# Performance work log

Hardware: AMD Instinct MI355X
Metric: run time of the kernel (lower is better)

The kernel has to match this reference:

```python
import jax, jax.numpy as jnp
import numpy as np

B, S, D, H = 2, 2048, 1024, 16
HD = D // H  # head_dim = 64


def setup_inputs() -> dict:
    key = jax.random.key(0)
    ks = jax.random.split(key, 9)
    s_in = 1.0 / np.sqrt(D)
    inp = {
        "hidden_state": jax.random.normal(ks[0], (B, S, D), dtype=jnp.float32),
        # per-head projections, stacked: [H, D, HD]
        "Wq": jax.random.uniform(ks[1], (H, D, HD), jnp.float32, -s_in, s_in),
        "bq": jax.random.uniform(ks[2], (H, HD), jnp.float32, -s_in, s_in),
        "Wk": jax.random.uniform(ks[3], (H, D, HD), jnp.float32, -s_in, s_in),
        "bk": jax.random.uniform(ks[4], (H, HD), jnp.float32, -s_in, s_in),
        "Wv": jax.random.uniform(ks[5], (H, D, HD), jnp.float32, -s_in, s_in),
        "bv": jax.random.uniform(ks[6], (H, HD), jnp.float32, -s_in, s_in),
        # output linear: [D, D]
        "Wo": jax.random.uniform(ks[7], (D, D), jnp.float32, -s_in, s_in),
        "bo": jax.random.uniform(ks[8], (D,), jnp.float32, -s_in, s_in),
    }
    return inp


def reference(hidden_state, Wq, bq, Wk, bk, Wv, bv, Wo, bo):
    # fused per-head projections: [B, H, S, HD]
    q = jnp.einsum("bsd,hde->bhse", hidden_state, Wq) + bq[None, :, None, :]
    k = jnp.einsum("bsd,hde->bhse", hidden_state, Wk) + bk[None, :, None, :]
    v = jnp.einsum("bsd,hde->bhse", hidden_state, Wv) + bv[None, :, None, :]
    scale = 1.0 / jnp.sqrt(jnp.float32(HD))
    scores = jnp.einsum("bhse,bhte->bhst", q, k) * scale  # [B, H, S, S]
    weights = jax.nn.softmax(scores, axis=-1)
    ctx = jnp.einsum("bhst,bhte->bhse", weights, v)       # [B, H, S, HD]
    # concat heads along last dim -> [B, S, D]
    ctx = jnp.transpose(ctx, (0, 2, 1, 3)).reshape(B, S, D)
    return ctx @ Wo + bo
```

## Files before the change

kernel.cpp:

```cpp
#include <hip/hip_runtime.h>
#include <hip/hip_bf16.h>
#include <math.h>

#define BB 2
#define SS 2048
#define DD 1024
#define HH 16
#define HD 64

typedef __attribute__((ext_vector_type(8))) _Float16 f16x8;
typedef __attribute__((ext_vector_type(2))) __fp16 fp16x2;
typedef __attribute__((ext_vector_type(8))) unsigned short u16x8;
typedef __attribute__((ext_vector_type(4))) float f32x4;
typedef __attribute__((ext_vector_type(4))) unsigned short u16x4;

__device__ __forceinline__ unsigned short hbits(_Float16 h) {
    union { _Float16 h; unsigned short s; } u; u.h = h; return u.s;
}

__device__ __forceinline__ int swz(int row, int grp) {
    return (row << 6) + (((grp) ^ (row & 7)) << 3);
}

__device__ __forceinline__ float fexp2(float x) {
#if __has_builtin(__builtin_amdgcn_exp2f)
    return __builtin_amdgcn_exp2f(x);
#else
    return exp2f(x);
#endif
}

__device__ __forceinline__ u16x4 pack4(float p0, float p1, float p2, float p3) {
#if __has_builtin(__builtin_amdgcn_cvt_pkrtz)
    union { fp16x2 h[2]; u16x4 u; } pu;
    pu.h[0] = __builtin_amdgcn_cvt_pkrtz(p0, p1);
    pu.h[1] = __builtin_amdgcn_cvt_pkrtz(p2, p3);
    return pu.u;
#else
    u16x4 r;
    r[0] = hbits((_Float16)p0); r[1] = hbits((_Float16)p1);
    r[2] = hbits((_Float16)p2); r[3] = hbits((_Float16)p3);
    return r;
#endif
}

__device__ __forceinline__ void gload_lds16(const unsigned short* g, unsigned short* l) {
#if __has_builtin(__builtin_amdgcn_global_load_lds)
    auto gp = (const __attribute__((address_space(1))) unsigned int*)(uintptr_t)g;
    auto lp = (__attribute__((address_space(3))) unsigned int*)(uintptr_t)l;
    __builtin_amdgcn_global_load_lds(gp, lp, 16, 0, 0);
#else
    *(u16x8*)(l + (threadIdx.x & 63) * 8) = *(const u16x8*)g;
#endif
}

__device__ __forceinline__ void wait4_barrier() {
    asm volatile("s_waitcnt vmcnt(4) lgkmcnt(0)\n\ts_barrier" ::: "memory");
}
__device__ __forceinline__ void wait6_barrier() {
    asm volatile("s_waitcnt vmcnt(6) lgkmcnt(0)\n\ts_barrier" ::: "memory");
}
__device__ __forceinline__ void wait0_barrier() {
    asm volatile("s_waitcnt vmcnt(0) lgkmcnt(0)\n\ts_barrier" ::: "memory");
}

__global__ __launch_bounds__(256) void prep_convert(
    const float* __restrict__ X,
    const float* __restrict__ Wq, const float* __restrict__ Wk,
    const float* __restrict__ Wv, const float* __restrict__ Wo,
    unsigned short* __restrict__ Xh, unsigned short* __restrict__ WT)
{
    __shared__ __align__(16) unsigned short LT[64 * 68];
    const int bid = blockIdx.x;
    const int tid = threadIdx.x;

    if (bid < 2048) {
        const int base = bid * 2048 + tid * 8;
        float4 a = *(const float4*)&X[base];
        float4 b = *(const float4*)&X[base + 4];
        u16x8 o;
        o[0] = hbits((_Float16)a.x); o[1] = hbits((_Float16)a.y);
        o[2] = hbits((_Float16)a.z); o[3] = hbits((_Float16)a.w);
        o[4] = hbits((_Float16)b.x); o[5] = hbits((_Float16)b.y);
        o[6] = hbits((_Float16)b.z); o[7] = hbits((_Float16)b.w);
        *(u16x8*)&Xh[base] = o;
        return;
    }

    const int t = bid - 2048;
    const float* src;
    size_t stride;
    int outRow0, kcol0;
    if (t < 768) {
        const int nt = t >> 4, ktile = t & 15;
        const int sel = nt >> 4, hh = nt & 15;
        const float* Ws = (sel == 0) ? Wq : ((sel == 1) ? Wk : Wv);
        src = Ws + (size_t)hh * (DD * HD) + (size_t)ktile * 64 * HD;
        stride = HD;
        outRow0 = nt * 64;
        kcol0 = ktile * 64;
    } else {
        const int tt = t - 768;
        const int nt = tt & 15, ktile = tt >> 4;
        src = Wo + (size_t)ktile * 64 * DD + nt * 64;
        stride = DD;
        outRow0 = 3072 + nt * 64;
        kcol0 = ktile * 64;
    }

    const int e = tid & 63, dq = tid >> 6;
#pragma unroll
    for (int p = 0; p < 16; p++) {
        const int dl = p * 4 + dq;
        LT[e * 68 + dl] = hbits((_Float16)src[(size_t)dl * stride + e]);
    }
    __syncthreads();
    const int eo = tid >> 2, d16 = (tid & 3) * 16;
#pragma unroll
    for (int j = 0; j < 4; j++) {
        *(ushort4*)&WT[(size_t)(outRow0 + eo) * DD + kcol0 + d16 + j * 4] =
            *(const ushort4*)&LT[eo * 68 + d16 + j * 4];
    }
}

#define GBM 128
#define GBN 128
#define GBK 64
#define NKT (DD / GBK)
#define QBK 32
#define QNKT (DD / QBK)

__global__ __launch_bounds__(256) void qkv_gemm(
    const unsigned short* __restrict__ Xh, const unsigned short* __restrict__ WT,
    const float* __restrict__ bq, const float* __restrict__ bk,
    const float* __restrict__ bv,
    unsigned short* __restrict__ qh, unsigned short* __restrict__ kh,
    unsigned short* __restrict__ vTs, unsigned int* __restrict__ kc2)
{
    __shared__ __align__(16) unsigned short As[3][8 * 512];
    __shared__ __align__(16) unsigned short Bs[3][8 * 512];

    const int tid = threadIdx.x;
    const int f  = blockIdx.y * 24 + blockIdx.x;
    const int fs = (f & 7) * 96 + (f >> 3);
    const int bx = fs % 24, by = fs / 24;
    const int m0 = by * GBM;
    const int n0 = bx * GBN;
    const int lane = tid & 63;
    const int w = tid >> 6;
    const int wm = w & 1, wn = w >> 1;
    const int l15 = lane & 15, quad = lane >> 4;
    const int kstart = (fs * 7) & (QNKT - 1);

    int g_off[2];
#pragma unroll
    for (int p = 0; p < 2; p++) {
        const int c = p * 4 + w;
        g_off[p] = (c * 16 + l15) * DD + quad * 8;
    }

    f32x4 acc[4][4];
#pragma unroll
    for (int i = 0; i < 4; i++)
#pragma unroll
        for (int j = 0; j < 4; j++) acc[i][j] = (f32x4){0.f, 0.f, 0.f, 0.f};

    const unsigned short* Abase = Xh + (size_t)m0 * DD;
    const unsigned short* Bbase = WT + (size_t)n0 * DD;

    {
        const int k0 = kstart * QBK;
        const int k1 = ((kstart + 1) & (QNKT - 1)) * QBK;
#pragma unroll
        for (int p = 0; p < 2; p++) {
            gload_lds16(Abase + g_off[p] + k0, &As[0][(p * 4 + w) * 512]);
            gload_lds16(Bbase + g_off[p] + k0, &Bs[0][(p * 4 + w) * 512]);
        }
#pragma unroll
        for (int p = 0; p < 2; p++) {
            gload_lds16(Abase + g_off[p] + k1, &As[1][(p * 4 + w) * 512]);
            gload_lds16(Bbase + g_off[p] + k1, &Bs[1][(p * 4 + w) * 512]);
        }
    }
    wait0_barrier();

    int cur = 0, pre = 2;
    for (int t = 0; t < QNKT; t++) {
        if (t + 2 < QNKT) {
            const int kt2 = ((kstart + t + 2) & (QNKT - 1)) * QBK;
#pragma unroll
            for (int p = 0; p < 2; p++) {
                gload_lds16(Abase + g_off[p] + kt2, &As[pre][(p * 4 + w) * 512]);
                gload_lds16(Bbase + g_off[p] + kt2, &Bs[pre][(p * 4 + w) * 512]);
            }
        }
        f16x8 af[4], bf[4];
#pragma unroll
        for (int i = 0; i < 4; i++) {
            af[i] = *(const f16x8*)&As[cur][(wm * 4 + i) * 512 + lane * 8];
            bf[i] = *(const f16x8*)&Bs[cur][(wn * 4 + i) * 512 + lane * 8];
        }
#pragma unroll
        for (int ns = 0; ns < 4; ns++)
#pragma unroll
            for (int ms = 0; ms < 4; ms++)
                acc[ms][ns] = __builtin_amdgcn_mfma_f32_16x16x32_f16(
                    af[ms], bf[ns], acc[ms][ns], 0, 0, 0);
        if (t < QNKT - 2)       wait4_barrier();
        else if (t == QNKT - 2) wait0_barrier();
        cur = (cur == 2) ? 0 : cur + 1;
        pre = (pre == 2) ? 0 : pre + 1;
    }

    const int sel = n0 >> 10;
    const int hw = ((n0 + wn * 64) >> 6) & 15;
    const int bblk = m0 >> 11;
    const float* bias = (sel == 0) ? bq : ((sel == 1) ? bk : bv);
    const size_t bh_base = ((size_t)bblk * HH + hw) * SS * HD;
    float wmx = 0.0f;
#pragma unroll
    for (int ms = 0; ms < 4; ms++) {
#pragma unroll
        for (int rr = 0; rr < 4; rr++) {
            const int m = m0 + wm * 64 + ms * 16 + quad * 4 + rr;
            const int s = m & (SS - 1);
            const int s63 = s & 63;
            float v2 = 0.0f;
#pragma unroll
            for (int ns = 0; ns < 4; ns++) {
                const int e = ns * 16 + l15;
                const float val = acc[ms][ns][rr] + bias[hw * HD + e];
                if (sel == 0) {
                    qh[bh_base + (size_t)s * HD + e] = hbits((_Float16)val);
                } else if (sel == 1) {
                    v2 = fmaf(val, val, v2);
                    const size_t kofs = bh_base + (size_t)(s >> 6) * 4096
                                      + swz(s63, e >> 3) + (e & 7);
                    kh[kofs] = hbits((_Float16)val);
                } else {
                    const size_t vofs = bh_base + (size_t)(s >> 6) * 4096
                                      + swz(e, s63 >> 3) + (s63 & 7);
                    vTs[vofs] = hbits((_Float16)val);
                }
            }
            if (sel == 1) {
                v2 += __shfl_xor(v2, 1);
                v2 += __shfl_xor(v2, 2);
                v2 += __shfl_xor(v2, 4);
                v2 += __shfl_xor(v2, 8);
                wmx = fmaxf(wmx, v2);
            }
        }
    }
    if (sel == 1) {
        wmx = fmaxf(wmx, __shfl_xor(wmx, 16));
        wmx = fmaxf(wmx, __shfl_xor(wmx, 32));
        if (lane == 0)
            atomicMax(&kc2[bblk * HH + hw], __float_as_uint(wmx));
    }
}

__global__ __launch_bounds__(256) void out_gemm(
    const unsigned short* __restrict__ Ctxh, const unsigned short* __restrict__ WoT,
    const float* __restrict__ bo, float* __restrict__ out)
{
    __shared__ __align__(16) unsigned short As[3][16 * 512];
    __shared__ __align__(16) unsigned short Bs[3][8 * 512];

    const int tid = threadIdx.x;
    const int f  = blockIdx.y * 16 + blockIdx.x;
    const int fs = (f & 7) * 64 + (f >> 3);
    const int bx = fs % 16, by = fs / 16;
    const int m0 = by * 128;
    const int n0 = bx * 64;
    const int lane = tid & 63;
    const int w = tid >> 6;
    const int wm = w & 1, wn = w >> 1;
    const int l15 = lane & 15, quad = lane >> 4;
    const int kstart = (fs * 5) & (NKT - 1);

    int g_off[4];
#pragma unroll
    for (int p = 0; p < 4; p++) {
        const int c = p * 4 + w;
        g_off[p] = ((c >> 1) * 16 + l15) * DD + (c & 1) * 32 + quad * 8;
    }

    f32x4 acc[4][2];
#pragma unroll
    for (int i = 0; i < 4; i++)
#pragma unroll
        for (int j = 0; j < 2; j++) acc[i][j] = (f32x4){0.f, 0.f, 0.f, 0.f};

    const unsigned short* Abase = Ctxh + (size_t)m0 * DD;
    const unsigned short* Bbase = WoT + (size_t)n0 * DD;

    {
        const int k0 = kstart * GBK;
        const int k1 = ((kstart + 1) & (NKT - 1)) * GBK;
#pragma unroll
        for (int p = 0; p < 4; p++)
            gload_lds16(Abase + g_off[p] + k0, &As[0][(p * 4 + w) * 512]);
#pragma unroll
        for (int p = 0; p < 2; p++)
            gload_lds16(Bbase + g_off[p] + k0, &Bs[0][(p * 4 + w) * 512]);
#pragma unroll
        for (int p = 0; p < 4; p++)
            gload_lds16(Abase + g_off[p] + k1, &As[1][(p * 4 + w) * 512]);
#pragma unroll
        for (int p = 0; p < 2; p++)
            gload_lds16(Bbase + g_off[p] + k1, &Bs[1][(p * 4 + w) * 512]);
    }
    wait0_barrier();

    int cur = 0, pre = 2;
    for (int it = 0; it < NKT; it++) {
        if (it + 2 < NKT) {
            const int kt2 = ((kstart + it + 2) & (NKT - 1)) * GBK;
#pragma unroll
            for (int p = 0; p < 4; p++)
                gload_lds16(Abase + g_off[p] + kt2, &As[pre][(p * 4 + w) * 512]);
#pragma unroll
            for (int p = 0; p < 2; p++)
                gload_lds16(Bbase + g_off[p] + kt2, &Bs[pre][(p * 4 + w) * 512]);
        }
#pragma unroll
        for (int ks = 0; ks < 2; ks++) {
            f16x8 af[4], bf[2];
#pragma unroll
            for (int i = 0; i < 4; i++)
                af[i] = *(const f16x8*)&As[cur][((wm * 4 + i) * 2 + ks) * 512 + lane * 8];
#pragma unroll
            for (int j = 0; j < 2; j++)
                bf[j] = *(const f16x8*)&Bs[cur][((wn * 2 + j) * 2 + ks) * 512 + lane * 8];
#pragma unroll
            for (int ns = 0; ns < 2; ns++)
#pragma unroll
                for (int ms = 0; ms < 4; ms++)
                    acc[ms][ns] = __builtin_amdgcn_mfma_f32_16x16x32_f16(
                        af[ms], bf[ns], acc[ms][ns], 0, 0, 0);
        }
        if (it < NKT - 2)       wait6_barrier();
        else if (it == NKT - 2) wait0_barrier();
        cur = (cur == 2) ? 0 : cur + 1;
        pre = (pre == 2) ? 0 : pre + 1;
    }

#pragma unroll
    for (int ms = 0; ms < 4; ms++) {
#pragma unroll
        for (int rr = 0; rr < 4; rr++) {
            const size_t m = (size_t)(m0 + wm * 64 + ms * 16 + quad * 4 + rr);
#pragma unroll
            for (int ns = 0; ns < 2; ns++) {
                const int n = n0 + wn * 32 + ns * 16 + l15;
                out[m * DD + n] = acc[ms][ns][rr] + bo[n];
            }
        }
    }
}

#define TQB 128
#define TKB 64
#define NT (SS / TKB)
#define C1 0.1803368801111204f

__global__ __launch_bounds__(256) void attn_mfma(
    const unsigned short* __restrict__ qh, const unsigned short* __restrict__ kh,
    const unsigned short* __restrict__ vTs, const unsigned int* __restrict__ kc2,
    unsigned short* __restrict__ ctxh)
{
    __shared__ __align__(16) unsigned short KL [3][TKB * 64];
    __shared__ __align__(16) unsigned short VtL[3][HD * 64];
    __shared__ __align__(16) unsigned short PsL[4][32 * 64];

    const int tid  = threadIdx.x;
    const int lane = tid & 63;
    const int w    = tid >> 6;
    const int l15  = lane & 15;
    const int quad = lane >> 4;
    const int f  = blockIdx.y * 16 + blockIdx.x;
    const int fs = (f & 7) * 64 + (f >> 3);
    const int bh = fs >> 4;
    const int q0 = (fs & 15) * TQB;
    const int t0 = (fs * 7) & (NT - 1);

    const float kfac = sqrtf(__uint_as_float(kc2[bh])) * 1.01f * C1;

    f16x8 qf[2][2];
    float M2[2];
#pragma unroll
    for (int msub = 0; msub < 2; msub++) {
        const unsigned short* qrow =
            qh + ((size_t)bh * SS + q0 + w * 32 + msub * 16 + l15) * HD;
        float nq2 = 0.0f;
#pragma unroll
        for (int dstep = 0; dstep < 2; dstep++) {
            qf[msub][dstep] = *(const f16x8*)&qrow[dstep * 32 + quad * 8];
#pragma unroll
            for (int j = 0; j < 8; j++) {
                const float x = (float)qf[msub][dstep][j];
                nq2 = fmaf(x, x, nq2);
            }
        }
        nq2 += __shfl_xor(nq2, 16);
        nq2 += __shfl_xor(nq2, 32);
        M2[msub] = sqrtf(nq2) * kfac;
    }

    f16x8 ones;
#pragma unroll
    for (int j = 0; j < 8; j++) ones[j] = (_Float16)1.0f;

    f32x4 o[2][4], lones[2];
#pragma unroll
    for (int ms = 0; ms < 2; ms++) {
        lones[ms] = (f32x4){0.f, 0.f, 0.f, 0.f};
#pragma unroll
        for (int e = 0; e < 4; e++) o[ms][e] = (f32x4){0.f, 0.f, 0.f, 0.f};
    }

    const unsigned short* kb0 = kh  + (size_t)bh * SS * HD;
    const unsigned short* vb0 = vTs + (size_t)bh * SS * HD;

    {
        const size_t u0 = (size_t)t0 * 4096;
        const size_t u1 = (size_t)((t0 + 1) & (NT - 1)) * 4096;
        gload_lds16(kb0 + u0 + tid * 8,        &KL [0][w * 512]);
        gload_lds16(kb0 + u0 + 2048 + tid * 8, &KL [0][2048 + w * 512]);
        gload_lds16(vb0 + u0 + tid * 8,        &VtL[0][w * 512]);
        gload_lds16(vb0 + u0 + 2048 + tid * 8, &VtL[0][2048 + w * 512]);
        gload_lds16(kb0 + u1 + tid * 8,        &KL [1][w * 512]);
        gload_lds16(kb0 + u1 + 2048 + tid * 8, &KL [1][2048 + w * 512]);
        gload_lds16(vb0 + u1 + tid * 8,        &VtL[1][w * 512]);
        gload_lds16(vb0 + u1 + 2048 + tid * 8, &VtL[1][2048 + w * 512]);
    }
    wait0_barrier();

    int cur = 0, pre = 2;
    for (int t = 0; t < NT; t++) {
        if (t + 2 < NT) {
            const size_t u = (size_t)((t0 + t + 2) & (NT - 1)) * 4096;
            const unsigned short* kb = kb0 + u;
            const unsigned short* vb = vb0 + u;
            gload_lds16(kb + tid * 8,        &KL [pre][w * 512]);
            gload_lds16(kb + 2048 + tid * 8, &KL [pre][2048 + w * 512]);
            gload_lds16(vb + tid * 8,        &VtL[pre][w * 512]);
            gload_lds16(vb + 2048 + tid * 8, &VtL[pre][2048 + w * 512]);
        }

        f32x4 sc[2][4];
        __builtin_amdgcn_s_setprio(1);
#pragma unroll
        for (int ksub = 0; ksub < 4; ksub++) {
            const int row = ksub * 16 + l15;
            f16x8 k0 = *(const f16x8*)&KL[cur][swz(row, quad)];
            f16x8 k1 = *(const f16x8*)&KL[cur][swz(row, 4 + quad)];
#pragma unroll
            for (int msub = 0; msub < 2; msub++) {
                f32x4 a = (f32x4){0.f, 0.f, 0.f, 0.f};
                a = __builtin_amdgcn_mfma_f32_16x16x32_f16(k0, qf[msub][0], a, 0, 0, 0);
                a = __builtin_amdgcn_mfma_f32_16x16x32_f16(k1, qf[msub][1], a, 0, 0, 0);
                sc[msub][ksub] = a;
            }
        }
        __builtin_amdgcn_s_setprio(0);

#pragma unroll
        for (int msub = 0; msub < 2; msub++) {
            const int prow = msub * 16 + l15;
#pragma unroll
            for (int ksub = 0; ksub < 4; ksub++) {
                const float p0 = fexp2(fmaf(sc[msub][ksub][0], C1, -M2[msub]));
                const float p1 = fexp2(fmaf(sc[msub][ksub][1], C1, -M2[msub]));
                const float p2 = fexp2(fmaf(sc[msub][ksub][2], C1, -M2[msub]));
                const float p3 = fexp2(fmaf(sc[msub][ksub][3], C1, -M2[msub]));
                *(u16x4*)&PsL[w][swz(prow, ksub * 2 + (quad >> 1)) + (quad & 1) * 4] =
                    pack4(p0, p1, p2, p3);
            }
        }

        __builtin_amdgcn_s_setprio(1);
#pragma unroll
        for (int kj = 0; kj < 2; kj++) {
            f16x8 pa[2];
#pragma unroll
            for (int msub = 0; msub < 2; msub++)
                pa[msub] = *(const f16x8*)&PsL[w][swz(msub * 16 + l15, kj * 4 + quad)];
            lones[0] = __builtin_amdgcn_mfma_f32_16x16x32_f16(pa[0], ones, lones[0], 0, 0, 0);
            lones[1] = __builtin_amdgcn_mfma_f32_16x16x32_f16(pa[1], ones, lones[1], 0, 0, 0);
#pragma unroll
            for (int esub = 0; esub < 4; esub++) {
                f16x8 vr = *(const f16x8*)&VtL[cur][swz(esub * 16 + l15, kj * 4 + quad)];
                o[0][esub] = __builtin_amdgcn_mfma_f32_16x16x32_f16(pa[0], vr, o[0][esub], 0, 0, 0);
                o[1][esub] = __builtin_amdgcn_mfma_f32_16x16x32_f16(pa[1], vr, o[1][esub], 0, 0, 0);
            }
        }
        __builtin_amdgcn_s_setprio(0);

        if (t < NT - 2)       wait4_barrier();
        else if (t == NT - 2) wait0_barrier();
        cur = (cur == 2) ? 0 : cur + 1;
        pre = (pre == 2) ? 0 : pre + 1;
    }

    const int b = bh >> 4;
    const int h = bh & 15;
#pragma unroll
    for (int msub = 0; msub < 2; msub++) {
#pragma unroll
        for (int rr = 0; rr < 4; rr++) {
            const float linv = 1.0f / lones[msub][rr];
            const int row = q0 + w * 32 + msub * 16 + quad * 4 + rr;
#pragma unroll
            for (int esub = 0; esub < 4; esub++) {
                ctxh[((size_t)b * SS + row) * DD + h * HD + esub * 16 + l15] =
                    hbits((_Float16)(o[msub][esub][rr] * linv));
            }
        }
    }
}

extern "C" void kernel_launch(void* const* d_in, const int* in_sizes, int n_in,
                              void* d_out, int out_size, void* d_ws, size_t ws_size,
                              hipStream_t stream) {
    const float* X  = (const float*)d_in[0];
    const float* Wq = (const float*)d_in[1];
    const float* bq = (const float*)d_in[2];
    const float* Wk = (const float*)d_in[3];
    const float* bk = (const float*)d_in[4];
    const float* Wv = (const float*)d_in[5];
    const float* bv = (const float*)d_in[6];
    const float* Wo = (const float*)d_in[7];
    const float* bo = (const float*)d_in[8];
    float* out = (float*)d_out;

    const size_t NB2 = (size_t)4096 * 1024 * 2;
    unsigned char* w8 = (unsigned char*)d_ws;
    unsigned short* Xh   = (unsigned short*)(w8);
    unsigned short* WT   = (unsigned short*)(w8 + NB2);
    unsigned short* qh   = (unsigned short*)(w8 + 2 * NB2);
    unsigned short* kh   = (unsigned short*)(w8 + 3 * NB2);
    unsigned short* vTs  = (unsigned short*)(w8 + 4 * NB2);
    unsigned short* ctxh = (unsigned short*)(w8 + 5 * NB2);
    unsigned int*   kc2  = (unsigned int*)(w8 + 6 * NB2);
    unsigned short* WoT  = WT + (size_t)3072 * 1024;

    (void)hipMemsetAsync(kc2, 0, BB * HH * sizeof(unsigned int), stream);

    prep_convert<<<dim3(3072), 256, 0, stream>>>(X, Wq, Wk, Wv, Wo, Xh, WT);

    qkv_gemm<<<dim3(3072 / GBN, 4096 / GBM), 256, 0, stream>>>(
        Xh, WT, bq, bk, bv, qh, kh, vTs, kc2);

    attn_mfma<<<dim3(SS / TQB, BB * HH), 256, 0, stream>>>(qh, kh, vTs, kc2, ctxh);

    out_gemm<<<dim3(1024 / 64, 4096 / 128), 256, 0, stream>>>(ctxh, WoT, bo, out);
}
```

Measured before the change: 225.7 us.

## Drop staggered K-start offsets and tile swizzle, add occupancy launch bounds

```diff
diff --git a/kernel.cpp b/kernel.cpp
--- a/kernel.cpp
+++ b/kernel.cpp
@@ -130,7 +130,7 @@
 #define QBK 32
 #define QNKT (DD / QBK)
 
-__global__ __launch_bounds__(256) void qkv_gemm(
+__global__ __launch_bounds__(256, 3) void qkv_gemm(
     const unsigned short* __restrict__ Xh, const unsigned short* __restrict__ WT,
     const float* __restrict__ bq, const float* __restrict__ bk,
     const float* __restrict__ bv,
@@ -141,16 +141,12 @@
     __shared__ __align__(16) unsigned short Bs[3][8 * 512];
 
     const int tid = threadIdx.x;
-    const int f  = blockIdx.y * 24 + blockIdx.x;
-    const int fs = (f & 7) * 96 + (f >> 3);
-    const int bx = fs % 24, by = fs / 24;
-    const int m0 = by * GBM;
-    const int n0 = bx * GBN;
+    const int m0 = blockIdx.y * GBM;
+    const int n0 = blockIdx.x * GBN;
     const int lane = tid & 63;
     const int w = tid >> 6;
     const int wm = w & 1, wn = w >> 1;
     const int l15 = lane & 15, quad = lane >> 4;
-    const int kstart = (fs * 7) & (QNKT - 1);
 
     int g_off[2];
 #pragma unroll
@@ -168,26 +164,22 @@
     const unsigned short* Abase = Xh + (size_t)m0 * DD;
     const unsigned short* Bbase = WT + (size_t)n0 * DD;
 
-    {
-        const int k0 = kstart * QBK;
-        const int k1 = ((kstart + 1) & (QNKT - 1)) * QBK;
-#pragma unroll
-        for (int p = 0; p < 2; p++) {
-            gload_lds16(Abase + g_off[p] + k0, &As[0][(p * 4 + w) * 512]);
-            gload_lds16(Bbase + g_off[p] + k0, &Bs[0][(p * 4 + w) * 512]);
-        }
-#pragma unroll
-        for (int p = 0; p < 2; p++) {
-            gload_lds16(Abase + g_off[p] + k1, &As[1][(p * 4 + w) * 512]);
-            gload_lds16(Bbase + g_off[p] + k1, &Bs[1][(p * 4 + w) * 512]);
-        }
+#pragma unroll
+    for (int p = 0; p < 2; p++) {
+        gload_lds16(Abase + g_off[p], &As[0][(p * 4 + w) * 512]);
+        gload_lds16(Bbase + g_off[p], &Bs[0][(p * 4 + w) * 512]);
+    }
+#pragma unroll
+    for (int p = 0; p < 2; p++) {
+        gload_lds16(Abase + g_off[p] + QBK, &As[1][(p * 4 + w) * 512]);
+        gload_lds16(Bbase + g_off[p] + QBK, &Bs[1][(p * 4 + w) * 512]);
     }
     wait0_barrier();
 
     int cur = 0, pre = 2;
     for (int t = 0; t < QNKT; t++) {
         if (t + 2 < QNKT) {
-            const int kt2 = ((kstart + t + 2) & (QNKT - 1)) * QBK;
+            const int kt2 = (t + 2) * QBK;
 #pragma unroll
             for (int p = 0; p < 2; p++) {
                 gload_lds16(Abase + g_off[p] + kt2, &As[pre][(p * 4 + w) * 512]);
@@ -260,7 +252,7 @@
     }
 }
 
-__global__ __launch_bounds__(256) void out_gemm(
+__global__ __launch_bounds__(256, 2) void out_gemm(
     const unsigned short* __restrict__ Ctxh, const unsigned short* __restrict__ WoT,
     const float* __restrict__ bo, float* __restrict__ out)
 {
@@ -277,7 +269,6 @@
     const int w = tid >> 6;
     const int wm = w & 1, wn = w >> 1;
     const int l15 = lane & 15, quad = lane >> 4;
-    const int kstart = (fs * 5) & (NKT - 1);
 
     int g_off[4];
 #pragma unroll
@@ -295,28 +286,24 @@
     const unsigned short* Abase = Ctxh + (size_t)m0 * DD;
     const unsigned short* Bbase = WoT + (size_t)n0 * DD;
 
-    {
-        const int k0 = kstart * GBK;
-        const int k1 = ((kstart + 1) & (NKT - 1)) * GBK;
-#pragma unroll
-        for (int p = 0; p < 4; p++)
-            gload_lds16(Abase + g_off[p] + k0, &As[0][(p * 4 + w) * 512]);
-#pragma unroll
-        for (int p = 0; p < 2; p++)
-            gload_lds16(Bbase + g_off[p] + k0, &Bs[0][(p * 4 + w) * 512]);
-#pragma unroll
-        for (int p = 0; p < 4; p++)
-            gload_lds16(Abase + g_off[p] + k1, &As[1][(p * 4 + w) * 512]);
-#pragma unroll
-        for (int p = 0; p < 2; p++)
-            gload_lds16(Bbase + g_off[p] + k1, &Bs[1][(p * 4 + w) * 512]);
-    }
+#pragma unroll
+    for (int p = 0; p < 4; p++)
+        gload_lds16(Abase + g_off[p], &As[0][(p * 4 + w) * 512]);
+#pragma unroll
+    for (int p = 0; p < 2; p++)
+        gload_lds16(Bbase + g_off[p], &Bs[0][(p * 4 + w) * 512]);
+#pragma unroll
+    for (int p = 0; p < 4; p++)
+        gload_lds16(Abase + g_off[p] + GBK, &As[1][(p * 4 + w) * 512]);
+#pragma unroll
+    for (int p = 0; p < 2; p++)
+        gload_lds16(Bbase + g_off[p] + GBK, &Bs[1][(p * 4 + w) * 512]);
     wait0_barrier();
 
     int cur = 0, pre = 2;
     for (int it = 0; it < NKT; it++) {
         if (it + 2 < NKT) {
-            const int kt2 = ((kstart + it + 2) & (NKT - 1)) * GBK;
+            const int kt2 = (it + 2) * GBK;
 #pragma unroll
             for (int p = 0; p < 4; p++)
                 gload_lds16(Abase + g_off[p] + kt2, &As[pre][(p * 4 + w) * 512]);
@@ -365,7 +352,7 @@
 #define NT (SS / TKB)
 #define C1 0.1803368801111204f
 
-__global__ __launch_bounds__(256) void attn_mfma(
+__global__ __launch_bounds__(256, 2) void attn_mfma(
     const unsigned short* __restrict__ qh, const unsigned short* __restrict__ kh,
     const unsigned short* __restrict__ vTs, const unsigned int* __restrict__ kc2,
     unsigned short* __restrict__ ctxh)
@@ -383,7 +370,6 @@
     const int fs = (f & 7) * 64 + (f >> 3);
     const int bh = fs >> 4;
     const int q0 = (fs & 15) * TQB;
-    const int t0 = (fs * 7) & (NT - 1);
 
     const float kfac = sqrtf(__uint_as_float(kc2[bh])) * 1.01f * C1;
 
@@ -423,26 +409,21 @@
     const unsigned short* kb0 = kh  + (size_t)bh * SS * HD;
     const unsigned short* vb0 = vTs + (size_t)bh * SS * HD;
 
-    {
-        const size_t u0 = (size_t)t0 * 4096;
-        const size_t u1 = (size_t)((t0 + 1) & (NT - 1)) * 4096;
-        gload_lds16(kb0 + u0 + tid * 8,        &KL [0][w * 512]);
-        gload_lds16(kb0 + u0 + 2048 + tid * 8, &KL [0][2048 + w * 512]);
-        gload_lds16(vb0 + u0 + tid * 8,        &VtL[0][w * 512]);
-        gload_lds16(vb0 + u0 + 2048 + tid * 8, &VtL[0][2048 + w * 512]);
-        gload_lds16(kb0 + u1 + tid * 8,        &KL [1][w * 512]);
-        gload_lds16(kb0 + u1 + 2048 + tid * 8, &KL [1][2048 + w * 512]);
-        gload_lds16(vb0 + u1 + tid * 8,        &VtL[1][w * 512]);
-        gload_lds16(vb0 + u1 + 2048 + tid * 8, &VtL[1][2048 + w * 512]);
-    }
+    gload_lds16(kb0 + tid * 8,        &KL [0][w * 512]);
+    gload_lds16(kb0 + 2048 + tid * 8, &KL [0][2048 + w * 512]);
+    gload_lds16(vb0 + tid * 8,        &VtL[0][w * 512]);
+    gload_lds16(vb0 + 2048 + tid * 8, &VtL[0][2048 + w * 512]);
+    gload_lds16(kb0 + 4096 + tid * 8, &KL [1][w * 512]);
+    gload_lds16(kb0 + 6144 + tid * 8, &KL [1][2048 + w * 512]);
+    gload_lds16(vb0 + 4096 + tid * 8, &VtL[1][w * 512]);
+    gload_lds16(vb0 + 6144 + tid * 8, &VtL[1][2048 + w * 512]);
     wait0_barrier();
 
     int cur = 0, pre = 2;
     for (int t = 0; t < NT; t++) {
         if (t + 2 < NT) {
-            const size_t u = (size_t)((t0 + t + 2) & (NT - 1)) * 4096;
-            const unsigned short* kb = kb0 + u;
-            const unsigned short* vb = vb0 + u;
+            const unsigned short* kb = kb0 + (size_t)(t + 2) * 4096;
+            const unsigned short* vb = vb0 + (size_t)(t + 2) * 4096;
             gload_lds16(kb + tid * 8,        &KL [pre][w * 512]);
             gload_lds16(kb + 2048 + tid * 8, &KL [pre][2048 + w * 512]);
             gload_lds16(vb + tid * 8,        &VtL[pre][w * 512]);
```

After: 222.8 us. No clear change (-1.3%).
